# Kernel optimization log

Measured on AMD Instinct MI355X. Metric: run time of the kernel, lower is better.

Reference implementation:

```python
import jax, jax.numpy as jnp
import numpy as np

KS = 3
PAD = 1
N = KS * KS  # 9 sampling points per output location


def setup_inputs() -> dict:
    key = jax.random.key(0)
    k1, k2, k3 = jax.random.split(key, 3)
    b, c, H, W, outc = 4, 128, 64, 64, 128
    x = jax.random.normal(k1, (b, c, H, W), jnp.float32)
    offset = jax.random.normal(k2, (b, 2 * N, H, W), jnp.float32)
    weight = jax.random.normal(k3, (outc, c, KS, KS), jnp.float32) * 0.05
    return {"x": x, "offset": offset, "weight": weight}


def reference(x, offset, weight):
    b, c, H, W = x.shape
    h, w = offset.shape[2], offset.shape[3]
    # reorder interleaved (x,y,x,y,...) offset channels to (all x, all y)
    idx = jnp.concatenate([jnp.arange(0, 2 * N, 2), jnp.arange(1, 2 * N, 2)])
    offset = offset[:, idx]
    # zero padding
    xp = jnp.pad(x, ((0, 0), (0, 0), (PAD, PAD), (PAD, PAD)))
    Hp, Wp = H + 2 * PAD, W + 2 * PAD
    # kernel-relative offsets p_n: [1, 2N, 1, 1]
    r = np.arange(-(KS - 1) // 2, (KS - 1) // 2 + 1)
    pnx, pny = np.meshgrid(r, r, indexing='ij')
    p_n = jnp.asarray(np.concatenate([pnx.flatten(), pny.flatten()]).reshape(1, 2 * N, 1, 1), jnp.float32)
    # base grid p_0: [1, 2N, h, w], coords start at 1 (padded frame)
    p0x, p0y = np.meshgrid(np.arange(1, h + 1), np.arange(1, w + 1), indexing='ij')
    p_0 = jnp.asarray(np.concatenate([np.tile(p0x.reshape(1, 1, h, w), (1, N, 1, 1)),
                                      np.tile(p0y.reshape(1, 1, h, w), (1, N, 1, 1))], axis=1), jnp.float32)
    p = jnp.transpose(p_0 + p_n + offset, (0, 2, 3, 1))  # [b, h, w, 2N]
    px, py = p[..., :N], p[..., N:]
    fx, fy = jnp.floor(px), jnp.floor(py)
    # 4 corner integer coords, clamped to padded image
    q_lt_x = jnp.clip(fx, 0, Hp - 1).astype(jnp.int32)
    q_lt_y = jnp.clip(fy, 0, Wp - 1).astype(jnp.int32)
    q_rb_x = jnp.clip(fx + 1, 0, Hp - 1).astype(jnp.int32)
    q_rb_y = jnp.clip(fy + 1, 0, Wp - 1).astype(jnp.int32)
    # out-of-range mask: snap p to floor(p) there (matches original, incl. zero grad thru floor)
    mask_x = jax.lax.stop_gradient(((px < PAD) | (px > Hp - 1 - PAD)).astype(px.dtype))
    mask_y = jax.lax.stop_gradient(((py < PAD) | (py > Wp - 1 - PAD)).astype(py.dtype))
    px = px * (1 - mask_x) + fx * mask_x
    py = py * (1 - mask_y) + fy * mask_y
    px = jnp.clip(px, 0, Hp - 1)
    py = jnp.clip(py, 0, Wp - 1)
    qltx = q_lt_x.astype(px.dtype); qlty = q_lt_y.astype(px.dtype)
    qrbx = q_rb_x.astype(px.dtype); qrby = q_rb_y.astype(px.dtype)
    # bilinear weights: [b, h, w, N]
    g_lt = (1 + (qltx - px)) * (1 + (qlty - py))
    g_rb = (1 - (qrbx - px)) * (1 - (qrby - py))
    g_lb = (1 + (qltx - px)) * (1 - (qrby - py))
    g_rt = (1 - (qrbx - px)) * (1 + (qlty - py))

    xv = xp.reshape(b, c, Hp * Wp)

    def gather(qx, qy):
        lin = (qx * Wp + qy).reshape(b, 1, h * w * N)
        g = jnp.take_along_axis(xv, jnp.broadcast_to(lin, (b, c, h * w * N)), axis=2)
        return g.reshape(b, c, h, w, N)

    x_off = (g_lt[:, None] * gather(q_lt_x, q_lt_y)
             + g_rb[:, None] * gather(q_rb_x, q_rb_y)
             + g_lb[:, None] * gather(q_lt_x, q_rb_y)
             + g_rt[:, None] * gather(q_rb_x, q_lt_y))  # [b, c, h, w, N]
    # N = i*ks + j -> out[(h,i),(w,j)]
    xo = x_off.reshape(b, c, h, w, KS, KS).transpose(0, 1, 2, 4, 3, 5).reshape(b, c, h * KS, w * KS)
    out = jax.lax.conv_general_dilated(xo, weight, window_strides=(KS, KS), padding='VALID',
                                       dimension_numbers=('NCHW', 'OIHW', 'NCHW'))
    return out
```

## Files before the change

### kernel.cpp

```cpp
#include <hip/hip_runtime.h>


typedef __bf16  v8bf16 __attribute__((ext_vector_type(8)));
typedef __bf16  bf16x2 __attribute__((ext_vector_type(2)));
typedef float   f32x4  __attribute__((ext_vector_type(4)));
typedef unsigned short ushort4v __attribute__((ext_vector_type(4)));
typedef _Float16 half4v __attribute__((ext_vector_type(4)));

#define CIN  128
#define NPT  9
#define KTOT 1152
#define OC   128
#define PX   32
#define NDESC (NPT * PX)
#define KSTEPS 36
#define KSC  12
#define LDBc 392
#define DTOT (9 * 4 * 64 * 64)
#define PXR  64
#define LDR  392

__global__ __launch_bounds__(256) void xpose_kernel(const float* __restrict__ x,
                                                    __bf16* __restrict__ xt) {
    __shared__ float tile[64][33];
    const int bidx = blockIdx.x;
    const int b   = bidx >> 8;
    const int hw0 = ((bidx >> 2) & 63) * 64;
    const int c0  = (bidx & 3) * 32;
    const int tid = threadIdx.x;
    #pragma unroll
    for (int r = 0; r < 8; ++r) {
        int c_l  = (tid >> 6) + r * 4;
        int hw_l = tid & 63;
        tile[hw_l][c_l] = x[((size_t)(b * CIN + c0 + c_l) << 12) + hw0 + hw_l];
    }
    __syncthreads();
    #pragma unroll
    for (int r = 0; r < 8; ++r) {
        int hw_l = (tid >> 5) + r * 8;
        int c_l  = tid & 31;
        xt[((size_t)(b * 4096 + hw0 + hw_l)) * CIN + c0 + c_l] = (__bf16)tile[hw_l][c_l];
    }
}

__global__ __launch_bounds__(256) void wfrag_kernel(const float* __restrict__ w,
                                                    __bf16* __restrict__ wfrag) {
    int t = blockIdx.x * 256 + threadIdx.x;
    if (t >= 8 * KSTEPS * 64) return;
    int lane = t & 63;
    int ks   = (t >> 6) % KSTEPS;
    int ot   = t / (KSTEPS * 64);
    int o    = ot * 16 + (lane & 15);
    v8bf16 frag;
    #pragma unroll
    for (int e = 0; e < 8; ++e) {
        int k   = ks * 32 + (lane >> 4) * 8 + e;
        int tap = k >> 7, c = k & 127;
        frag[e] = (__bf16)w[(size_t)o * KTOT + c * NPT + tap];
    }
    *(v8bf16*)(wfrag + (size_t)t * 8) = frag;
}

__global__ __launch_bounds__(256) void desc_kernel(const float* __restrict__ off,
                                                   uint4* __restrict__ desc) {
    int t = blockIdx.x * 256 + threadIdx.x;
    if (t >= DTOT) return;
    int j   = t & 63;
    int i   = (t >> 6) & 63;
    int b   = (t >> 12) & 3;
    int tap = t >> 14;

    float ox = off[(((b * 18) + 2 * tap) << 12) + (i << 6) + j];
    float oy = off[(((b * 18) + 2 * tap + 1) << 12) + (i << 6) + j];
    float px = (float)(i + tap / 3) + ox;
    float py = (float)(j + tap % 3) + oy;
    float fx = floorf(px), fy = floorf(py);
    int qltx = (int)fminf(fmaxf(fx, 0.f), 65.f);
    int qlty = (int)fminf(fmaxf(fy, 0.f), 65.f);
    int qrbx = (int)fminf(fmaxf(fx + 1.f, 0.f), 65.f);
    int qrby = (int)fminf(fmaxf(fy + 1.f, 0.f), 65.f);
    if (px < 1.f || px > 64.f) px = fx;
    if (py < 1.f || py > 64.f) py = fy;
    px = fminf(fmaxf(px, 0.f), 65.f);
    py = fminf(fmaxf(py, 0.f), 65.f);
    float wxl = 1.f + (float)qltx - px;
    float wxr = 1.f - ((float)qrbx - px);
    float wyl = 1.f + (float)qlty - py;
    float wyr = 1.f - ((float)qrby - py);
    float g[4] = { wxl * wyl, wxr * wyr, wxl * wyr, wxr * wyl };
    int qx[4] = { qltx, qrbx, qltx, qrbx };
    int qy[4] = { qlty, qrby, qrby, qlty };
    unsigned short idx[4];
    half4v gh;
    #pragma unroll
    for (int cr = 0; cr < 4; ++cr) {
        bool inb = (qx[cr] >= 1) && (qx[cr] <= 64) && (qy[cr] >= 1) && (qy[cr] <= 64);
        idx[cr] = inb ? (unsigned short)((qx[cr] - 1) * 64 + (qy[cr] - 1)) : 0;
        gh[cr]  = inb ? (_Float16)g[cr] : (_Float16)0.f;
    }
    uint4 rec;
    rec.x = (unsigned)idx[0] | ((unsigned)idx[1] << 16);
    rec.y = (unsigned)idx[2] | ((unsigned)idx[3] << 16);
    __builtin_memcpy(&rec.z, &gh, 8);
    int d = (((b << 6) + i) * 64 + j) * 9 + tap;
    desc[d] = rec;
}

__global__ __launch_bounds__(512, 6) void splitk_kernel(
    const uint4* __restrict__ desc, const __bf16* __restrict__ xt,
    const __bf16* __restrict__ wfrag, float* __restrict__ part)
{
    __shared__ __align__(16) __bf16 Bt[PXR][LDR];

    const int bidx = blockIdx.x;
    const int kh  = bidx & 3 ? 0 : 0;
    const int kh3 = bidx % 3;
    const int rest = bidx / 3;
    const int i   = rest & 63;
    const int b   = rest >> 6;
    const int tid = threadIdx.x;
    (void)kh;

    const int tap0 = kh3 * 3;

    const int l  = tid & 63;
    const int wv = tid >> 6;

    const __bf16* xtb = xt + (((size_t)b << 12) * CIN);
    const int pix_base = ((b << 6) + i) * 64;

    #pragma unroll 4
    for (int dd = 0; dd < 24; ++dd) {
        int dl = wv * 24 + dd;
        int tap_l = dl >> 6, p = dl & 63;
        int d = (pix_base + p) * 9 + tap0 + tap_l;
        uint4 q = desc[d];
        unsigned short idx[4] = { (unsigned short)(q.x & 0xffff), (unsigned short)(q.x >> 16),
                                  (unsigned short)(q.y & 0xffff), (unsigned short)(q.y >> 16) };
        half4v gh;
        __builtin_memcpy(&gh, &q.z, 8);
        float s0 = 0.f, s1 = 0.f;
        #pragma unroll
        for (int cr = 0; cr < 4; ++cr) {
            unsigned int v = *(const unsigned int*)(xtb + (size_t)idx[cr] * CIN + 2 * l);
            float c0v, c1v;
            unsigned int lo = v << 16, hi = v & 0xffff0000u;
            __builtin_memcpy(&c0v, &lo, 4);
            __builtin_memcpy(&c1v, &hi, 4);
            float gf = (float)gh[cr];
            s0 += gf * c0v;
            s1 += gf * c1v;
        }
        bf16x2 pr = { (__bf16)s0, (__bf16)s1 };
        *(bf16x2*)&Bt[p][tap_l * CIN + 2 * l] = pr;
    }
    __syncthreads();

    const int quad = l >> 4;
    const int lr   = l & 15;

    f32x4 acc0 = {0.f, 0.f, 0.f, 0.f};
    f32x4 acc1 = {0.f, 0.f, 0.f, 0.f};
    f32x4 acc2 = {0.f, 0.f, 0.f, 0.f};
    f32x4 acc3 = {0.f, 0.f, 0.f, 0.f};

    const __bf16* brow0 = &Bt[lr][quad * 8];
    const __bf16* brow1 = &Bt[16 + lr][quad * 8];
    const __bf16* brow2 = &Bt[32 + lr][quad * 8];
    const __bf16* brow3 = &Bt[48 + lr][quad * 8];

    #pragma unroll 3
    for (int ks = 0; ks < KSC; ++ks) {
        int ks_g = kh3 * KSC + ks;
        v8bf16 afrag = *(const v8bf16*)(wfrag + (((size_t)wv * KSTEPS + ks_g) * 64 + l) * 8);
        v8bf16 b0 = *(const v8bf16*)(brow0 + ks * 32);
        v8bf16 b1 = *(const v8bf16*)(brow1 + ks * 32);
        v8bf16 b2 = *(const v8bf16*)(brow2 + ks * 32);
        v8bf16 b3 = *(const v8bf16*)(brow3 + ks * 32);
        acc0 = __builtin_amdgcn_mfma_f32_16x16x32_bf16(afrag, b0, acc0, 0, 0, 0);
        acc1 = __builtin_amdgcn_mfma_f32_16x16x32_bf16(afrag, b1, acc1, 0, 0, 0);
        acc2 = __builtin_amdgcn_mfma_f32_16x16x32_bf16(afrag, b2, acc2, 0, 0, 0);
        acc3 = __builtin_amdgcn_mfma_f32_16x16x32_bf16(afrag, b3, acc3, 0, 0, 0);
    }

    float* pc = part + ((size_t)kh3 << 21);
    int obase = wv * 16 + quad * 4;
    float* opb = pc + (((size_t)(b * OC + obase)) << 12) + (i << 6) + lr;
    #pragma unroll
    for (int ph = 0; ph < 4; ++ph) {
        f32x4 a = (ph == 0) ? acc0 : (ph == 1) ? acc1 : (ph == 2) ? acc2 : acc3;
        float* op = opb + ph * 16;
        #pragma unroll
        for (int r = 0; r < 4; ++r)
            op[(size_t)r << 12] = a[r];
    }
}

__global__ __launch_bounds__(256) void reduce_kernel(const float* __restrict__ part,
                                                     float* __restrict__ out) {
    int t = blockIdx.x * 256 + threadIdx.x;
    f32x4 a = *(const f32x4*)(part + (size_t)t * 4);
    f32x4 c = *(const f32x4*)(part + (1u << 21) + (size_t)t * 4);
    f32x4 d = *(const f32x4*)(part + (2u << 21) + (size_t)t * 4);
    f32x4 r = a + c + d;
    *(f32x4*)(out + (size_t)t * 4) = r;
}

__global__ __launch_bounds__(512, 8) void deform_fused_kernel(
    const float* __restrict__ x, const float* __restrict__ off,
    const float* __restrict__ w, const __bf16* __restrict__ wfrag,
    const __bf16* __restrict__ xt, float* __restrict__ out, int mode)
{
    __shared__ __align__(16) __bf16 Bt[PX][LDBc];
    __shared__ __align__(8)  unsigned short sIdxP[NDESC][4];
    __shared__ __align__(8)  _Float16      sGP[NDESC][4];

    const int bidx = blockIdx.x;
    const int b   = bidx >> 8;
    const int i   = (bidx >> 2) & 63;
    const int j0  = ((bidx >> 1) & 1) * PX;
    const int oh  = bidx & 1;
    const int tid = threadIdx.x;

    if (tid < NDESC) {
        int k = tid >> 5, p = tid & 31;
        int j = j0 + p;
        float ox = off[(((b * 18) + 2 * k) * 64 + i) * 64 + j];
        float oy = off[(((b * 18) + 2 * k + 1) * 64 + i) * 64 + j];
        float px = (float)(i + k / 3) + ox;
        float py = (float)(j + k % 3) + oy;
        float fx = floorf(px), fy = floorf(py);
        int qltx = (int)fminf(fmaxf(fx, 0.f), 65.f);
        int qlty = (int)fminf(fmaxf(fy, 0.f), 65.f);
        int qrbx = (int)fminf(fmaxf(fx + 1.f, 0.f), 65.f);
        int qrby = (int)fminf(fmaxf(fy + 1.f, 0.f), 65.f);
        if (px < 1.f || px > 64.f) px = fx;
        if (py < 1.f || py > 64.f) py = fy;
        px = fminf(fmaxf(px, 0.f), 65.f);
        py = fminf(fmaxf(py, 0.f), 65.f);
        float wxl = 1.f + (float)qltx - px;
        float wxr = 1.f - ((float)qrbx - px);
        float wyl = 1.f + (float)qlty - py;
        float wyr = 1.f - ((float)qrby - py);
        float g[4] = { wxl * wyl, wxr * wyr, wxl * wyr, wxr * wyl };
        int qx[4] = { qltx, qrbx, qltx, qrbx };
        int qy[4] = { qlty, qrby, qrby, qlty };
        #pragma unroll
        for (int cr = 0; cr < 4; ++cr) {
            bool inb = (qx[cr] >= 1) && (qx[cr] <= 64) && (qy[cr] >= 1) && (qy[cr] <= 64);
            sIdxP[tid][cr] = inb ? (unsigned short)((qx[cr] - 1) * 64 + (qy[cr] - 1)) : 0;
            sGP[tid][cr]   = inb ? (_Float16)g[cr] : (_Float16)0.f;
        }
    }
    __syncthreads();

    const int l    = tid & 63;
    const int wv   = tid >> 6;
    const int ot   = oh * 4 + (wv & 3);
    const int ph   = wv >> 2;
    const int quad = l >> 4;
    const int lr   = l & 15;

    f32x4 acc = {0.f, 0.f, 0.f, 0.f};
    const __bf16* xtb = xt + ((size_t)b * 4096) * CIN;
    const float*  xb  = x + ((size_t)b * CIN << 12);
    const __bf16* brow = &Bt[ph * 16 + lr][quad * 8];

    for (int t = 0; t < 3; ++t) {
        if (mode == 2) {
            #pragma unroll 4
            for (int dd = 0; dd < KSC; ++dd) {
                int dl = wv * KSC + dd;
                int tap_l = dl >> 5, p = dl & 31;
                int d = t * 96 + dl;
                ushort4v id = *(const ushort4v*)&sIdxP[d][0];
                half4v   gh = *(const half4v*)&sGP[d][0];
                float s0 = 0.f, s1 = 0.f;
                #pragma unroll
                for (int cr = 0; cr < 4; ++cr) {
                    unsigned int v = *(const unsigned int*)(xtb + (size_t)id[cr] * CIN + 2 * l);
                    float c0v, c1v;
                    unsigned int lo = v << 16, hi = v & 0xffff0000u;
                    __builtin_memcpy(&c0v, &lo, 4);
                    __builtin_memcpy(&c1v, &hi, 4);
                    float gf = (float)gh[cr];
                    s0 += gf * c0v;
                    s1 += gf * c1v;
                }
                bf16x2 pr = { (__bf16)s0, (__bf16)s1 };
                *(bf16x2*)&Bt[p][tap_l * CIN + 2 * l] = pr;
            }
        } else {
            for (int dd = 0; dd < KSC; ++dd) {
                int dl = wv * KSC + dd;
                int tap_l = dl >> 5, p = dl & 31;
                int d = t * 96 + dl;
                ushort4v id = *(const ushort4v*)&sIdxP[d][0];
                half4v   gh = *(const half4v*)&sGP[d][0];
                float s0 = 0.f, s1 = 0.f;
                #pragma unroll
                for (int cr = 0; cr < 4; ++cr) {
                    float gf = (float)gh[cr];
                    s0 += gf * xb[((size_t)(2 * l) << 12) + id[cr]];
                    s1 += gf * xb[((size_t)(2 * l + 1) << 12) + id[cr]];
                }
                bf16x2 pr = { (__bf16)s0, (__bf16)s1 };
                *(bf16x2*)&Bt[p][tap_l * CIN + 2 * l] = pr;
            }
        }
        __syncthreads();

        #pragma unroll 4
        for (int ks = 0; ks < KSC; ++ks) {
            int ks_g = t * KSC + ks;
            v8bf16 bfrag = *(const v8bf16*)(brow + ks * 32);
            v8bf16 afrag;
            if (mode >= 1) {
                afrag = *(const v8bf16*)(wfrag + (((size_t)ot * KSTEPS + ks_g) * 64 + l) * 8);
            } else {
                int o = ot * 16 + lr;
                #pragma unroll
                for (int e = 0; e < 8; ++e) {
                    int k = ks_g * 32 + quad * 8 + e;
                    int tap = k >> 7, c = k & 127;
                    afrag[e] = (__bf16)w[(size_t)o * KTOT + c * NPT + tap];
                }
            }
            acc = __builtin_amdgcn_mfma_f32_16x16x32_bf16(afrag, bfrag, acc, 0, 0, 0);
        }
        if (t < 2) __syncthreads();
    }

    {
        int obase = ot * 16 + quad * 4;
        float* op = out + (((size_t)(b * OC + obase)) << 12) + (i << 6) + j0 + ph * 16 + lr;
        #pragma unroll
        for (int r = 0; r < 4; ++r)
            op[(size_t)r << 12] = acc[r];
    }
}

extern "C" void kernel_launch(void* const* d_in, const int* in_sizes, int n_in,
                              void* d_out, int out_size, void* d_ws, size_t ws_size,
                              hipStream_t stream) {
    const float* x   = (const float*)d_in[0];
    const float* off = (const float*)d_in[1];
    const float* w   = (const float*)d_in[2];
    float* out = (float*)d_out;

    const size_t wfrag_bytes = (size_t)OC * KTOT * sizeof(__bf16);
    const size_t xt_bytes    = (size_t)4 * 4096 * CIN * sizeof(__bf16);
    const size_t desc_bytes  = (size_t)DTOT * 16;
    const size_t part_bytes  = (size_t)3 * 4 * OC * 4096 * sizeof(float);

    int mode = 0;
    if (ws_size >= wfrag_bytes + xt_bytes + desc_bytes + part_bytes) mode = 3;
    else if (ws_size >= wfrag_bytes + xt_bytes) mode = 2;
    else if (ws_size >= wfrag_bytes) mode = 1;

    __bf16* wfrag = (__bf16*)d_ws;
    __bf16* xt    = (__bf16*)((char*)d_ws + wfrag_bytes);
    uint4*  desc  = (uint4*) ((char*)d_ws + wfrag_bytes + xt_bytes);
    float*  part  = (float*) ((char*)d_ws + wfrag_bytes + xt_bytes + desc_bytes);

    if (mode >= 1)
        wfrag_kernel<<<(8 * KSTEPS * 64 + 255) / 256, 256, 0, stream>>>(w, wfrag);
    if (mode >= 2)
        xpose_kernel<<<4 * 64 * 4, 256, 0, stream>>>(x, xt);

    if (mode == 3) {
        desc_kernel<<<(DTOT + 255) / 256, 256, 0, stream>>>(off, desc);
        splitk_kernel<<<4 * 64 * 3, 512, 0, stream>>>(desc, xt, wfrag, part);
        reduce_kernel<<<2048, 256, 0, stream>>>(part, out);
    } else {
        deform_fused_kernel<<<4 * 64 * 2 * 2, 512, 0, stream>>>(x, off, w, wfrag, xt, out, mode);
    }
}
```

Baseline: 94.20 us.

## Merge prep kernels into one launch and replace split-K reduce with atomics

Folds the weight-fragment, transpose and descriptor kernels, plus zeroing of the output, into a single prep kernel dispatched by block range. The split-K partial buffer and its reduce kernel go away: each split now adds its result straight into the output with unsafe float atomics. The gather loop also has each lane load four bf16 channels instead of two, so one wave covers two pixels per iteration. This saves two launches and the partial-buffer write and read traffic, at the cost of atomic contention and a summation order that is no longer deterministic.

```diff
diff --git a/kernel.cpp b/kernel.cpp
--- a/kernel.cpp
+++ b/kernel.cpp
@@ -3,6 +3,7 @@
 
 typedef __bf16  v8bf16 __attribute__((ext_vector_type(8)));
 typedef __bf16  bf16x2 __attribute__((ext_vector_type(2)));
+typedef __bf16  bf16x4 __attribute__((ext_vector_type(4)));
 typedef float   f32x4  __attribute__((ext_vector_type(4)));
 typedef unsigned short ushort4v __attribute__((ext_vector_type(4)));
 typedef _Float16 half4v __attribute__((ext_vector_type(4)));
@@ -20,51 +21,14 @@
 #define PXR  64
 #define LDR  392
 
-__global__ __launch_bounds__(256) void xpose_kernel(const float* __restrict__ x,
-                                                    __bf16* __restrict__ xt) {
-    __shared__ float tile[64][33];
-    const int bidx = blockIdx.x;
-    const int b   = bidx >> 8;
-    const int hw0 = ((bidx >> 2) & 63) * 64;
-    const int c0  = (bidx & 3) * 32;
-    const int tid = threadIdx.x;
-    #pragma unroll
-    for (int r = 0; r < 8; ++r) {
-        int c_l  = (tid >> 6) + r * 4;
-        int hw_l = tid & 63;
-        tile[hw_l][c_l] = x[((size_t)(b * CIN + c0 + c_l) << 12) + hw0 + hw_l];
-    }
-    __syncthreads();
-    #pragma unroll
-    for (int r = 0; r < 8; ++r) {
-        int hw_l = (tid >> 5) + r * 8;
-        int c_l  = tid & 31;
-        xt[((size_t)(b * 4096 + hw0 + hw_l)) * CIN + c0 + c_l] = (__bf16)tile[hw_l][c_l];
-    }
-}
-
-__global__ __launch_bounds__(256) void wfrag_kernel(const float* __restrict__ w,
-                                                    __bf16* __restrict__ wfrag) {
-    int t = blockIdx.x * 256 + threadIdx.x;
-    if (t >= 8 * KSTEPS * 64) return;
-    int lane = t & 63;
-    int ks   = (t >> 6) % KSTEPS;
-    int ot   = t / (KSTEPS * 64);
-    int o    = ot * 16 + (lane & 15);
-    v8bf16 frag;
-    #pragma unroll
-    for (int e = 0; e < 8; ++e) {
-        int k   = ks * 32 + (lane >> 4) * 8 + e;
-        int tap = k >> 7, c = k & 127;
-        frag[e] = (__bf16)w[(size_t)o * KTOT + c * NPT + tap];
-    }
-    *(v8bf16*)(wfrag + (size_t)t * 8) = frag;
-}
-
-__global__ __launch_bounds__(256) void desc_kernel(const float* __restrict__ off,
-                                                   uint4* __restrict__ desc) {
-    int t = blockIdx.x * 256 + threadIdx.x;
-    if (t >= DTOT) return;
+#define PB_WFRAG 72
+#define PB_XPOSE 1024
+#define PB_DESC  576
+#define PB_ZERO  2048
+#define PB_TOTAL (PB_WFRAG + PB_XPOSE + PB_DESC + PB_ZERO)
+
+__device__ __forceinline__ void desc_compute(const float* __restrict__ off, int t,
+                                             uint4* __restrict__ desc) {
     int j   = t & 63;
     int i   = (t >> 6) & 63;
     int b   = (t >> 12) & 3;
@@ -106,20 +70,72 @@
     desc[d] = rec;
 }
 
+__global__ __launch_bounds__(256) void prep_kernel(
+    const float* __restrict__ x, const float* __restrict__ off,
+    const float* __restrict__ w, __bf16* __restrict__ wfrag,
+    __bf16* __restrict__ xt, uint4* __restrict__ desc,
+    float* __restrict__ out)
+{
+    __shared__ float tile[64][33];
+    const int bid = blockIdx.x;
+    const int tid = threadIdx.x;
+
+    if (bid < PB_WFRAG) {
+        int t = bid * 256 + tid;
+        if (t < 8 * KSTEPS * 64) {
+            int lane = t & 63;
+            int ks   = (t >> 6) % KSTEPS;
+            int ot   = t / (KSTEPS * 64);
+            int o    = ot * 16 + (lane & 15);
+            v8bf16 frag;
+            #pragma unroll
+            for (int e = 0; e < 8; ++e) {
+                int k   = ks * 32 + (lane >> 4) * 8 + e;
+                int tap = k >> 7, c = k & 127;
+                frag[e] = (__bf16)w[(size_t)o * KTOT + c * NPT + tap];
+            }
+            *(v8bf16*)(wfrag + (size_t)t * 8) = frag;
+        }
+    } else if (bid < PB_WFRAG + PB_XPOSE) {
+        const int bidx = bid - PB_WFRAG;
+        const int b   = bidx >> 8;
+        const int hw0 = ((bidx >> 2) & 63) * 64;
+        const int c0  = (bidx & 3) * 32;
+        #pragma unroll
+        for (int r = 0; r < 8; ++r) {
+            int c_l  = (tid >> 6) + r * 4;
+            int hw_l = tid & 63;
+            tile[hw_l][c_l] = x[((size_t)(b * CIN + c0 + c_l) << 12) + hw0 + hw_l];
+        }
+        __syncthreads();
+        #pragma unroll
+        for (int r = 0; r < 8; ++r) {
+            int hw_l = (tid >> 5) + r * 8;
+            int c_l  = tid & 31;
+            xt[((size_t)(b * 4096 + hw0 + hw_l)) * CIN + c0 + c_l] = (__bf16)tile[hw_l][c_l];
+        }
+    } else if (bid < PB_WFRAG + PB_XPOSE + PB_DESC) {
+        int t = (bid - PB_WFRAG - PB_XPOSE) * 256 + tid;
+        if (t < DTOT) desc_compute(off, t, desc);
+    } else {
+        int t = (bid - PB_WFRAG - PB_XPOSE - PB_DESC) * 256 + tid;
+        f32x4 z = {0.f, 0.f, 0.f, 0.f};
+        *(f32x4*)(out + (size_t)t * 4) = z;
+    }
+}
+
 __global__ __launch_bounds__(512, 6) void splitk_kernel(
     const uint4* __restrict__ desc, const __bf16* __restrict__ xt,
-    const __bf16* __restrict__ wfrag, float* __restrict__ part)
+    const __bf16* __restrict__ wfrag, float* __restrict__ out)
 {
     __shared__ __align__(16) __bf16 Bt[PXR][LDR];
 
     const int bidx = blockIdx.x;
-    const int kh  = bidx & 3 ? 0 : 0;
     const int kh3 = bidx % 3;
     const int rest = bidx / 3;
     const int i   = rest & 63;
     const int b   = rest >> 6;
     const int tid = threadIdx.x;
-    (void)kh;
 
     const int tap0 = kh3 * 3;
 
@@ -129,9 +145,11 @@
     const __bf16* xtb = xt + (((size_t)b << 12) * CIN);
     const int pix_base = ((b << 6) + i) * 64;
 
-    #pragma unroll 4
-    for (int dd = 0; dd < 24; ++dd) {
-        int dl = wv * 24 + dd;
+    const int hh = l >> 5;
+    const int ll = l & 31;
+    #pragma unroll 3
+    for (int m = 0; m < 12; ++m) {
+        int dl = wv * 24 + 2 * m + hh;
         int tap_l = dl >> 6, p = dl & 63;
         int d = (pix_base + p) * 9 + tap0 + tap_l;
         uint4 q = desc[d];
@@ -139,20 +157,25 @@
                                   (unsigned short)(q.y & 0xffff), (unsigned short)(q.y >> 16) };
         half4v gh;
         __builtin_memcpy(&gh, &q.z, 8);
-        float s0 = 0.f, s1 = 0.f;
+        float s0 = 0.f, s1 = 0.f, s2 = 0.f, s3 = 0.f;
         #pragma unroll
         for (int cr = 0; cr < 4; ++cr) {
-            unsigned int v = *(const unsigned int*)(xtb + (size_t)idx[cr] * CIN + 2 * l);
-            float c0v, c1v;
-            unsigned int lo = v << 16, hi = v & 0xffff0000u;
-            __builtin_memcpy(&c0v, &lo, 4);
-            __builtin_memcpy(&c1v, &hi, 4);
+            uint2 v = *(const uint2*)(xtb + (size_t)idx[cr] * CIN + 4 * ll);
+            float c0v, c1v, c2v, c3v;
+            unsigned int l0 = v.x << 16, h0 = v.x & 0xffff0000u;
+            unsigned int l1 = v.y << 16, h1 = v.y & 0xffff0000u;
+            __builtin_memcpy(&c0v, &l0, 4);
+            __builtin_memcpy(&c1v, &h0, 4);
+            __builtin_memcpy(&c2v, &l1, 4);
+            __builtin_memcpy(&c3v, &h1, 4);
             float gf = (float)gh[cr];
             s0 += gf * c0v;
             s1 += gf * c1v;
-        }
-        bf16x2 pr = { (__bf16)s0, (__bf16)s1 };
-        *(bf16x2*)&Bt[p][tap_l * CIN + 2 * l] = pr;
+            s2 += gf * c2v;
+            s3 += gf * c3v;
+        }
+        bf16x4 pr = { (__bf16)s0, (__bf16)s1, (__bf16)s2, (__bf16)s3 };
+        *(bf16x4*)&Bt[p][tap_l * CIN + 4 * ll] = pr;
     }
     __syncthreads();
 
@@ -183,27 +206,16 @@
         acc3 = __builtin_amdgcn_mfma_f32_16x16x32_bf16(afrag, b3, acc3, 0, 0, 0);
     }
 
-    float* pc = part + ((size_t)kh3 << 21);
     int obase = wv * 16 + quad * 4;
-    float* opb = pc + (((size_t)(b * OC + obase)) << 12) + (i << 6) + lr;
+    float* opb = out + (((size_t)(b * OC + obase)) << 12) + (i << 6) + lr;
     #pragma unroll
     for (int ph = 0; ph < 4; ++ph) {
         f32x4 a = (ph == 0) ? acc0 : (ph == 1) ? acc1 : (ph == 2) ? acc2 : acc3;
         float* op = opb + ph * 16;
         #pragma unroll
         for (int r = 0; r < 4; ++r)
-            op[(size_t)r << 12] = a[r];
-    }
-}
-
-__global__ __launch_bounds__(256) void reduce_kernel(const float* __restrict__ part,
-                                                     float* __restrict__ out) {
-    int t = blockIdx.x * 256 + threadIdx.x;
-    f32x4 a = *(const f32x4*)(part + (size_t)t * 4);
-    f32x4 c = *(const f32x4*)(part + (1u << 21) + (size_t)t * 4);
-    f32x4 d = *(const f32x4*)(part + (2u << 21) + (size_t)t * 4);
-    f32x4 r = a + c + d;
-    *(f32x4*)(out + (size_t)t * 4) = r;
+            unsafeAtomicAdd(op + ((size_t)r << 12), a[r]);
+    }
 }
 
 __global__ __launch_bounds__(512, 8) void deform_fused_kernel(
@@ -340,6 +352,47 @@
     }
 }
 
+__global__ __launch_bounds__(256) void wfrag_kernel(const float* __restrict__ w,
+                                                    __bf16* __restrict__ wfrag) {
+    int t = blockIdx.x * 256 + threadIdx.x;
+    if (t >= 8 * KSTEPS * 64) return;
+    int lane = t & 63;
+    int ks   = (t >> 6) % KSTEPS;
+    int ot   = t / (KSTEPS * 64);
+    int o    = ot * 16 + (lane & 15);
+    v8bf16 frag;
+    #pragma unroll
+    for (int e = 0; e < 8; ++e) {
+        int k   = ks * 32 + (lane >> 4) * 8 + e;
+        int tap = k >> 7, c = k & 127;
+        frag[e] = (__bf16)w[(size_t)o * KTOT + c * NPT + tap];
+    }
+    *(v8bf16*)(wfrag + (size_t)t * 8) = frag;
+}
+
+__global__ __launch_bounds__(256) void xpose_kernel(const float* __restrict__ x,
+                                                    __bf16* __restrict__ xt) {
+    __shared__ float tile[64][33];
+    const int bidx = blockIdx.x;
+    const int b   = bidx >> 8;
+    const int hw0 = ((bidx >> 2) & 63) * 64;
+    const int c0  = (bidx & 3) * 32;
+    const int tid = threadIdx.x;
+    #pragma unroll
+    for (int r = 0; r < 8; ++r) {
+        int c_l  = (tid >> 6) + r * 4;
+        int hw_l = tid & 63;
+        tile[hw_l][c_l] = x[((size_t)(b * CIN + c0 + c_l) << 12) + hw0 + hw_l];
+    }
+    __syncthreads();
+    #pragma unroll
+    for (int r = 0; r < 8; ++r) {
+        int hw_l = (tid >> 5) + r * 8;
+        int c_l  = tid & 31;
+        xt[((size_t)(b * 4096 + hw0 + hw_l)) * CIN + c0 + c_l] = (__bf16)tile[hw_l][c_l];
+    }
+}
+
 extern "C" void kernel_launch(void* const* d_in, const int* in_sizes, int n_in,
                               void* d_out, int out_size, void* d_ws, size_t ws_size,
                               hipStream_t stream) {
@@ -351,28 +404,24 @@
     const size_t wfrag_bytes = (size_t)OC * KTOT * sizeof(__bf16);
     const size_t xt_bytes    = (size_t)4 * 4096 * CIN * sizeof(__bf16);
     const size_t desc_bytes  = (size_t)DTOT * 16;
-    const size_t part_bytes  = (size_t)3 * 4 * OC * 4096 * sizeof(float);
 
     int mode = 0;
-    if (ws_size >= wfrag_bytes + xt_bytes + desc_bytes + part_bytes) mode = 3;
+    if (ws_size >= wfrag_bytes + xt_bytes + desc_bytes) mode = 3;
     else if (ws_size >= wfrag_bytes + xt_bytes) mode = 2;
     else if (ws_size >= wfrag_bytes) mode = 1;
 
     __bf16* wfrag = (__bf16*)d_ws;
     __bf16* xt    = (__bf16*)((char*)d_ws + wfrag_bytes);
     uint4*  desc  = (uint4*) ((char*)d_ws + wfrag_bytes + xt_bytes);
-    float*  part  = (float*) ((char*)d_ws + wfrag_bytes + xt_bytes + desc_bytes);
-
-    if (mode >= 1)
-        wfrag_kernel<<<(8 * KSTEPS * 64 + 255) / 256, 256, 0, stream>>>(w, wfrag);
-    if (mode >= 2)
-        xpose_kernel<<<4 * 64 * 4, 256, 0, stream>>>(x, xt);
 
     if (mode == 3) {
-        desc_kernel<<<(DTOT + 255) / 256, 256, 0, stream>>>(off, desc);
-        splitk_kernel<<<4 * 64 * 3, 512, 0, stream>>>(desc, xt, wfrag, part);
-        reduce_kernel<<<2048, 256, 0, stream>>>(part, out);
+        prep_kernel<<<PB_TOTAL, 256, 0, stream>>>(x, off, w, wfrag, xt, desc, out);
+        splitk_kernel<<<4 * 64 * 3, 512, 0, stream>>>(desc, xt, wfrag, out);
     } else {
+        if (mode >= 1)
+            wfrag_kernel<<<(8 * KSTEPS * 64 + 255) / 256, 256, 0, stream>>>(w, wfrag);
+        if (mode >= 2)
+            xpose_kernel<<<4 * 64 * 4, 256, 0, stream>>>(x, xt);
         deform_fused_kernel<<<4 * 64 * 2 * 2, 512, 0, stream>>>(x, off, w, wfrag, xt, out, mode);
     }
 }
```

Result: slower. 101.7 us (+7.9%).
